# Optimization experiments

Measured on AMD Instinct MI355X. Metric: run time of the kernel, lower is better.

The kernel has to match this reference:

```python
import jax, jax.numpy as jnp
import numpy as np

D_MODEL = 1024
N_HEADS = 16
HEAD_DIM = D_MODEL // N_HEADS
B, LQ, LK = 4, 2048, 2048


def _rope(x, cos, sin):
    # x: (B, H, L, d); cos/sin: (B, 1, L, d)
    d = x.shape[-1]
    x1, x2 = x[..., : d // 2], x[..., d // 2 :]
    rotated = jnp.concatenate([-x2, x1], axis=-1)
    return x * cos + rotated * sin


def setup_inputs() -> dict:
    key = jax.random.key(0)
    ks = jax.random.split(key, 16)
    s = 1.0 / np.sqrt(D_MODEL)
    inp = {
        "query": jax.random.normal(ks[0], (B, LQ, D_MODEL), jnp.float32),
        "key": jax.random.normal(ks[1], (B, LK, D_MODEL), jnp.float32),
        "value": jax.random.normal(ks[2], (B, LK, D_MODEL), jnp.float32),
        "cos_q": jax.random.normal(ks[3], (B, LQ, HEAD_DIM), jnp.float32),
        "sin_q": jax.random.normal(ks[4], (B, LQ, HEAD_DIM), jnp.float32),
        "cos_k": jax.random.normal(ks[5], (B, LK, HEAD_DIM), jnp.float32),
        "sin_k": jax.random.normal(ks[6], (B, LK, HEAD_DIM), jnp.float32),
        "key_padding_mask": jnp.zeros((B, LK), dtype=bool),
        "Wq": jax.random.normal(ks[7], (D_MODEL, D_MODEL), jnp.float32) * s,
        "bq": jnp.zeros((D_MODEL,), jnp.float32),
        "Wk": jax.random.normal(ks[8], (D_MODEL, D_MODEL), jnp.float32) * s,
        "bk": jnp.zeros((D_MODEL,), jnp.float32),
        "Wv": jax.random.normal(ks[9], (D_MODEL, D_MODEL), jnp.float32) * s,
        "bv": jnp.zeros((D_MODEL,), jnp.float32),
        "Wo": jax.random.normal(ks[10], (D_MODEL, D_MODEL), jnp.float32) * s,
        "bo": jnp.zeros((D_MODEL,), jnp.float32),
    }
    return inp


def reference(query, key, value, cos_q, sin_q, cos_k, sin_k, key_padding_mask,
              Wq, bq, Wk, bk, Wv, bv, Wo, bo):
    Bq, Lq, _ = query.shape
    Lk = key.shape[1]
    scale = HEAD_DIM ** -0.5

    def proj(x, W, b, L):
        # torch Linear: x @ W.T + b, then (B, L, H, d) -> (B, H, L, d)
        y = jnp.einsum('ble,de->bld', x, W) + b
        return y.reshape(Bq, L, N_HEADS, HEAD_DIM).transpose(0, 2, 1, 3)

    q = proj(query, Wq, bq, Lq)
    k = proj(key, Wk, bk, Lk)
    v = proj(value, Wv, bv, Lk)

    q = _rope(q, cos_q[:, None, :Lq, :HEAD_DIM], sin_q[:, None, :Lq, :HEAD_DIM])
    k = _rope(k, cos_k[:, None, :Lk, :HEAD_DIM], sin_k[:, None, :Lk, :HEAD_DIM])

    attn = jnp.einsum('bhqd,bhkd->bhqk', q, k) * scale
    attn = jnp.where(key_padding_mask[:, None, None, :], -jnp.inf, attn)
    attn = jax.nn.softmax(attn, axis=-1)

    out = jnp.einsum('bhqk,bhkd->bhqd', attn, v)
    out = out.transpose(0, 2, 1, 3).reshape(Bq, Lq, D_MODEL)
    return jnp.einsum('ble,de->bld', out, Wo) + bo
```

## Files before the change

kernel.cpp:

```cpp
#include <hip/hip_runtime.h>
#include <hip/hip_bf16.h>
#include <stdint.h>
#include <stddef.h>

#define B_DIM 4
#define NH    16
#define LSEQ  2048
#define HD    64
#define DM    1024
#define TOKENS (B_DIM * LSEQ)

typedef __bf16 bf16_t;
typedef __attribute__((ext_vector_type(8))) __bf16 bf16x8;
typedef __attribute__((ext_vector_type(4))) __bf16 bf16x4;
typedef __attribute__((ext_vector_type(4))) float  f32x4;

#define GLD16(gp, lp) \
  __builtin_amdgcn_global_load_lds((__attribute__((address_space(1))) void*)(gp), \
                                   (__attribute__((address_space(3))) void*)(lp), 16, 0, 0)

__device__ __forceinline__ f32x4 mfma_16x16x32(bf16x8 a, bf16x8 b, f32x4 c) {
  return __builtin_amdgcn_mfma_f32_16x16x32_bf16(a, b, c, 0, 0, 0);
}

__global__ __launch_bounds__(256) void cast3_kernel(const float* __restrict__ a,
                                                    const float* __restrict__ b,
                                                    const float* __restrict__ c,
                                                    bf16_t* __restrict__ dst, int n) {
  const float* src = (blockIdx.y == 0) ? a : (blockIdx.y == 1) ? b : c;
  const int i = (blockIdx.x * 256 + threadIdx.x) * 4;
  if (i < n) {
    const float4 v = *(const float4*)(src + i);
    bf16x4 o;
    o[0] = (bf16_t)v.x; o[1] = (bf16_t)v.y; o[2] = (bf16_t)v.z; o[3] = (bf16_t)v.w;
    *(bf16x4*)(dst + (size_t)blockIdx.y * n + i) = o;
  }
}

__global__ __launch_bounds__(256) void cast4_kernel(const float* __restrict__ a,
                                                    const float* __restrict__ b,
                                                    const float* __restrict__ c,
                                                    const float* __restrict__ d,
                                                    bf16_t* __restrict__ dst, int n) {
  const float* src = (blockIdx.y == 0) ? a : (blockIdx.y == 1) ? b
                   : (blockIdx.y == 2) ? c : d;
  const int i = (blockIdx.x * 256 + threadIdx.x) * 4;
  if (i < n) {
    const float4 v = *(const float4*)(src + i);
    bf16x4 o;
    o[0] = (bf16_t)v.x; o[1] = (bf16_t)v.y; o[2] = (bf16_t)v.z; o[3] = (bf16_t)v.w;
    *(bf16x4*)(dst + (size_t)blockIdx.y * n + i) = o;
  }
}

__global__ __launch_bounds__(256) void qkv_proj_kernel(const bf16_t* __restrict__ X,
                                                       const bf16_t* __restrict__ Wb,
                                                       const float* __restrict__ bq,
                                                       const float* __restrict__ bk,
                                                       const float* __restrict__ bv,
                                                       const float* __restrict__ cos_q,
                                                       const float* __restrict__ sin_q,
                                                       const float* __restrict__ cos_k,
                                                       const float* __restrict__ sin_k,
                                                       bf16_t* __restrict__ qtb,
                                                       bf16_t* __restrict__ ktb,
                                                       bf16_t* __restrict__ vtb) {
  __shared__ bf16_t As[128 * 32];
  __shared__ bf16_t Bs[128 * 32];
  const int z = blockIdx.z;
  const bf16_t* A  = X  + (size_t)z * TOKENS * DM;
  const bf16_t* Bw = Wb + (size_t)z * DM * DM;
  const float* bias = (z == 0) ? bq : (z == 1) ? bk : bv;

  const int tid  = threadIdx.x;
  const int wave = tid >> 6, lane = tid & 63;
  const int quad = lane >> 4, l16 = lane & 15;
  const int m0 = blockIdx.x * 128, n0 = blockIdx.y * 128;
  const int wm = (wave >> 1) * 64, wn = (wave & 1) * 64;

  f32x4 acc[4][4];
#pragma unroll
  for (int i = 0; i < 4; ++i)
#pragma unroll
    for (int j = 0; j < 4; ++j) acc[i][j] = (f32x4){0.f, 0.f, 0.f, 0.f};

  const int srow = lane >> 2;
  const int scol = (lane & 3) * 8;

  for (int kk = 0; kk < DM; kk += 32) {
    __syncthreads();
#pragma unroll
    for (int t = 0; t < 2; ++t) {
      const int c   = wave * 2 + t;
      const int row = c * 16 + srow;
      GLD16(A  + (size_t)(m0 + row) * DM + kk + scol, As + c * 512);
      GLD16(Bw + (size_t)(n0 + row) * DM + kk + scol, Bs + c * 512);
    }
    __syncthreads();
    bf16x8 af[4], bfr[4];
#pragma unroll
    for (int i = 0; i < 4; ++i)
      af[i] = *(const bf16x8*)(As + (wm + i * 16 + l16) * 32 + quad * 8);
#pragma unroll
    for (int j = 0; j < 4; ++j)
      bfr[j] = *(const bf16x8*)(Bs + (wn + j * 16 + l16) * 32 + quad * 8);
#pragma unroll
    for (int i = 0; i < 4; ++i)
#pragma unroll
      for (int j = 0; j < 4; ++j)
        acc[i][j] = mfma_16x16x32(af[i], bfr[j], acc[i][j]);
  }

  if (z < 2) {
    const float* cosb = (z == 0) ? cos_q : cos_k;
    const float* sinb = (z == 0) ? sin_q : sin_k;
    bf16_t* out = (z == 0) ? qtb : ktb;
    const int h = (n0 + wn) >> 6;
#pragma unroll
    for (int i = 0; i < 4; ++i) {
#pragma unroll
      for (int j = 0; j < 2; ++j) {
        const int hd1 = j * 16 + l16;
        const int hd2 = hd1 + 32;
        const float bn1 = bias[n0 + wn + hd1];
        const float bn2 = bias[n0 + wn + hd2];
#pragma unroll
        for (int r = 0; r < 4; ++r) {
          const int m = m0 + wm + i * 16 + quad * 4 + r;
          const int b = m >> 11, l = m & (LSEQ - 1);
          const size_t cb = ((size_t)b * LSEQ + l) * HD;
          const float x1 = (float)(bf16_t)(acc[i][j][r] + bn1);
          const float x2 = (float)(bf16_t)(acc[i][j + 2][r] + bn2);
          const float c1 = cosb[cb + hd1], s1 = sinb[cb + hd1];
          const float c2 = cosb[cb + hd2], s2 = sinb[cb + hd2];
          bf16_t* dst = out + (((size_t)(b * NH + h)) * LSEQ + l) * HD;
          dst[hd1] = (bf16_t)(x1 * c1 - x2 * s1);
          dst[hd2] = (bf16_t)(x2 * c2 + x1 * s2);
        }
      }
    }
  } else {
#pragma unroll
    for (int i = 0; i < 4; ++i) {
      const int mb = m0 + wm + i * 16 + quad * 4;
      const int b = mb >> 11, l = mb & (LSEQ - 1);
#pragma unroll
      for (int j = 0; j < 4; ++j) {
        const int n = n0 + wn + j * 16 + l16;
        const int h = n >> 6, hd = n & (HD - 1);
        const float bn = bias[n];
        bf16x4 pk;
#pragma unroll
        for (int r = 0; r < 4; ++r) pk[r] = (bf16_t)(acc[i][j][r] + bn);
        *(bf16x4*)(vtb + (((size_t)(b * NH + h)) * HD + hd) * LSEQ + l) = pk;
      }
    }
  }
}

__global__ __launch_bounds__(256) void out_gemm_kernel(const bf16_t* __restrict__ A,
                                                       const bf16_t* __restrict__ Bw,
                                                       const float* __restrict__ bias,
                                                       float* __restrict__ out) {
  __shared__ bf16_t As[128 * 32];
  __shared__ bf16_t Bs[128 * 32];
  const int tid  = threadIdx.x;
  const int wave = tid >> 6, lane = tid & 63;
  const int quad = lane >> 4, l16 = lane & 15;
  const int m0 = blockIdx.x * 128, n0 = blockIdx.y * 128;
  const int wm = (wave >> 1) * 64, wn = (wave & 1) * 64;

  f32x4 acc[4][4];
#pragma unroll
  for (int i = 0; i < 4; ++i)
#pragma unroll
    for (int j = 0; j < 4; ++j) acc[i][j] = (f32x4){0.f, 0.f, 0.f, 0.f};

  const int srow = lane >> 2;
  const int scol = (lane & 3) * 8;

  for (int kk = 0; kk < DM; kk += 32) {
    __syncthreads();
#pragma unroll
    for (int t = 0; t < 2; ++t) {
      const int c   = wave * 2 + t;
      const int row = c * 16 + srow;
      GLD16(A  + (size_t)(m0 + row) * DM + kk + scol, As + c * 512);
      GLD16(Bw + (size_t)(n0 + row) * DM + kk + scol, Bs + c * 512);
    }
    __syncthreads();
    bf16x8 af[4], bfr[4];
#pragma unroll
    for (int i = 0; i < 4; ++i)
      af[i] = *(const bf16x8*)(As + (wm + i * 16 + l16) * 32 + quad * 8);
#pragma unroll
    for (int j = 0; j < 4; ++j)
      bfr[j] = *(const bf16x8*)(Bs + (wn + j * 16 + l16) * 32 + quad * 8);
#pragma unroll
    for (int i = 0; i < 4; ++i)
#pragma unroll
      for (int j = 0; j < 4; ++j)
        acc[i][j] = mfma_16x16x32(af[i], bfr[j], acc[i][j]);
  }

#pragma unroll
  for (int i = 0; i < 4; ++i)
#pragma unroll
    for (int j = 0; j < 4; ++j) {
      const int n  = n0 + wn + j * 16 + l16;
      const float bn = bias[n];
#pragma unroll
      for (int r = 0; r < 4; ++r) {
        const int m = m0 + wm + i * 16 + quad * 4 + r;
        out[(size_t)m * DM + n] = acc[i][j][r] + bn;
      }
    }
}

__global__ __launch_bounds__(256) void attn_kernel(const bf16_t* __restrict__ qt,
                                                   const bf16_t* __restrict__ kt,
                                                   const bf16_t* __restrict__ vt,
                                                   const unsigned char* __restrict__ mask,
                                                   bf16_t* __restrict__ ctx) {
  __shared__ bf16_t Kl[64 * 64];
  __shared__ bf16_t Vl[64 * 64];
  __shared__ bf16_t Pl[4 * 16 * 72];
  const int bh = blockIdx.y;
  const int b = bh >> 4, h = bh & (NH - 1);
  const int q0 = blockIdx.x * 128;
  const int tid = threadIdx.x;
  const int wave = tid >> 6, lane = tid & 63;
  const int quad = lane >> 4, l16 = lane & 15;
  const float scale_l2e = 0.125f * 1.44269504f;

  bf16x8 qa[2][2];
#pragma unroll
  for (int u = 0; u < 2; ++u) {
    const bf16_t* qrow = qt + (((size_t)bh * LSEQ) + q0 + wave * 32 + u * 16 + l16) * HD;
    qa[u][0] = *(const bf16x8*)(qrow + quad * 8);
    qa[u][1] = *(const bf16x8*)(qrow + 32 + quad * 8);
  }

  f32x4 O[2][4];
  float l_part[2][4];
#pragma unroll
  for (int u = 0; u < 2; ++u)
#pragma unroll
    for (int j = 0; j < 4; ++j) { O[u][j] = (f32x4){0.f, 0.f, 0.f, 0.f}; l_part[u][j] = 0.f; }

  const bf16_t* kbase = kt + (size_t)bh * LSEQ * HD;
  const bf16_t* vbase = vt + (size_t)bh * HD * LSEQ;
  const unsigned char* mrow = mask + (size_t)b * LSEQ;

  const int srow = lane >> 3;
  const int scb  = lane & 7;
  bf16_t* Plw = Pl + wave * 16 * 72;

  for (int k0 = 0; k0 < LSEQ; k0 += 64) {
    __syncthreads();
#pragma unroll
    for (int t = 0; t < 2; ++t) {
      const int c   = wave * 2 + t;
      const int row = c * 8 + srow;
      const int gcb = scb ^ (row & 7);
      GLD16(kbase + (size_t)(k0 + row) * HD + gcb * 8, Kl + c * 512);
      GLD16(vbase + (size_t)row * LSEQ + k0 + gcb * 8, Vl + c * 512);
    }
    __syncthreads();

    float mb[4];
#pragma unroll
    for (int j = 0; j < 4; ++j)
      mb[j] = mrow[k0 + j * 16 + l16] ? -__builtin_inff() : 0.f;

    f32x4 S[2][4];
#pragma unroll
    for (int j = 0; j < 4; ++j) {
      const int row = j * 16 + l16;
      const int sw  = row & 7;
      const bf16x8 kb0 = *(const bf16x8*)(Kl + row * 64 + ((quad)     ^ sw) * 8);
      const bf16x8 kb1 = *(const bf16x8*)(Kl + row * 64 + ((quad + 4) ^ sw) * 8);
#pragma unroll
      for (int u = 0; u < 2; ++u) {
        f32x4 a = (f32x4){0.f, 0.f, 0.f, 0.f};
        a = mfma_16x16x32(qa[u][0], kb0, a);
        a = mfma_16x16x32(qa[u][1], kb1, a);
#pragma unroll
        for (int r = 0; r < 4; ++r) {
          const float e = __builtin_amdgcn_exp2f(fmaf(a[r], scale_l2e, mb[j]));
          S[u][j][r] = e;
          l_part[u][r] += e;
        }
      }
    }

    bf16x8 pa[2][2];
#pragma unroll
    for (int u = 0; u < 2; ++u) {
#pragma unroll
      for (int j = 0; j < 4; ++j)
#pragma unroll
        for (int r = 0; r < 4; ++r)
          Plw[(quad * 4 + r) * 72 + j * 16 + l16] = (bf16_t)S[u][j][r];
      pa[u][0] = *(const bf16x8*)(Plw + l16 * 72 + quad * 8);
      pa[u][1] = *(const bf16x8*)(Plw + l16 * 72 + 32 + quad * 8);
    }

#pragma unroll
    for (int jd = 0; jd < 4; ++jd) {
      const int vrow = jd * 16 + l16;
      const int sw   = vrow & 7;
      const bf16x8 vb0 = *(const bf16x8*)(Vl + vrow * 64 + ((quad)     ^ sw) * 8);
      const bf16x8 vb1 = *(const bf16x8*)(Vl + vrow * 64 + ((quad + 4) ^ sw) * 8);
#pragma unroll
      for (int u = 0; u < 2; ++u) {
        O[u][jd] = mfma_16x16x32(pa[u][0], vb0, O[u][jd]);
        O[u][jd] = mfma_16x16x32(pa[u][1], vb1, O[u][jd]);
      }
    }
  }

#pragma unroll
  for (int u = 0; u < 2; ++u)
#pragma unroll
    for (int r = 0; r < 4; ++r) {
      float s = l_part[u][r];
#pragma unroll
      for (int off = 1; off < 16; off <<= 1) s += __shfl_xor(s, off);
      l_part[u][r] = 1.0f / s;
    }

#pragma unroll
  for (int u = 0; u < 2; ++u)
#pragma unroll
    for (int jd = 0; jd < 4; ++jd)
#pragma unroll
      for (int r = 0; r < 4; ++r) {
        const int l = q0 + wave * 32 + u * 16 + quad * 4 + r;
        const int d = h * HD + jd * 16 + l16;
        const float o = O[u][jd][r] * l_part[u][r];
        ctx[((size_t)b * LSEQ + l) * DM + d] = (bf16_t)o;
      }
}

extern "C" void kernel_launch(void* const* d_in, const int* in_sizes, int n_in,
                              void* d_out, int out_size, void* d_ws, size_t ws_size,
                              hipStream_t stream) {
  (void)in_sizes; (void)n_in; (void)out_size; (void)ws_size;
  const float* query = (const float*)d_in[0];
  const float* key   = (const float*)d_in[1];
  const float* value = (const float*)d_in[2];
  const float* cos_q = (const float*)d_in[3];
  const float* sin_q = (const float*)d_in[4];
  const float* cos_k = (const float*)d_in[5];
  const float* sin_k = (const float*)d_in[6];
  const unsigned char* mask = (const unsigned char*)d_in[7];
  const float* Wq = (const float*)d_in[8];
  const float* bq = (const float*)d_in[9];
  const float* Wk = (const float*)d_in[10];
  const float* bk = (const float*)d_in[11];
  const float* Wv = (const float*)d_in[12];
  const float* bv = (const float*)d_in[13];
  const float* Wo = (const float*)d_in[14];
  const float* bo = (const float*)d_in[15];
  float* out = (float*)d_out;

  const size_t ACT = (size_t)TOKENS * DM;
  const size_t WEL = (size_t)DM * DM;

  bf16_t* p   = (bf16_t*)d_ws;
  bf16_t* xq  = p; p += ACT;
  bf16_t* xk  = p; p += ACT;
  bf16_t* xv  = p; p += ACT;
  bf16_t* wqb = p; p += WEL;
  bf16_t* wkb = p; p += WEL;
  bf16_t* wvb = p; p += WEL;
  bf16_t* wob = p; p += WEL;
  bf16_t* qtb = p; p += ACT;
  bf16_t* ktb = p; p += ACT;
  bf16_t* vtb = p; p += ACT;
  bf16_t* ctx = xk;
  (void)xv; (void)wkb; (void)wvb;

  cast3_kernel<<<dim3((int)(ACT / 1024), 3), 256, 0, stream>>>(query, key, value, xq, (int)ACT);
  cast4_kernel<<<dim3((int)(WEL / 1024), 4), 256, 0, stream>>>(Wq, Wk, Wv, Wo, wqb, (int)WEL);

  qkv_proj_kernel<<<dim3(TOKENS / 128, DM / 128, 3), 256, 0, stream>>>(
      xq, wqb, bq, bk, bv, cos_q, sin_q, cos_k, sin_k, qtb, ktb, vtb);

  attn_kernel<<<dim3(LSEQ / 128, B_DIM * NH), 256, 0, stream>>>(qtb, ktb, vtb, mask, ctx);

  out_gemm_kernel<<<dim3(TOKENS / 128, DM / 128), 256, 0, stream>>>(ctx, wob, bo, out);
}
```

Before: 392.6 us.

## Double-buffer K/V tiles and keep softmax probabilities in registers

The attention kernel now double-buffers the K and V tiles in shared memory, prefetching the next tile while the current one is computed, so each step needs one barrier instead of two. It swaps the MFMA operand order so the score tile comes out transposed, and permutes the K rows on load so the probabilities can be packed straight into the PV operand without a round trip through shared memory. The mask becomes a wave-uniform check that is skipped when a 64-key tile has no masked keys, and the row-sum reduction is simplified. The extra buffer doubles the K/V shared-memory footprint and the occupancy hint adds register pressure.

```diff
diff --git a/kernel.cpp b/kernel.cpp
--- a/kernel.cpp
+++ b/kernel.cpp
@@ -217,14 +217,13 @@
     }
 }
 
-__global__ __launch_bounds__(256) void attn_kernel(const bf16_t* __restrict__ qt,
-                                                   const bf16_t* __restrict__ kt,
-                                                   const bf16_t* __restrict__ vt,
-                                                   const unsigned char* __restrict__ mask,
-                                                   bf16_t* __restrict__ ctx) {
-  __shared__ bf16_t Kl[64 * 64];
-  __shared__ bf16_t Vl[64 * 64];
-  __shared__ bf16_t Pl[4 * 16 * 72];
+__global__ __launch_bounds__(256, 4) void attn_kernel(const bf16_t* __restrict__ qt,
+                                                      const bf16_t* __restrict__ kt,
+                                                      const bf16_t* __restrict__ vt,
+                                                      const unsigned char* __restrict__ mask,
+                                                      bf16_t* __restrict__ ctx) {
+  __shared__ bf16_t Kl[2][64 * 64];
+  __shared__ bf16_t Vl[2][64 * 64];
   const int bh = blockIdx.y;
   const int b = bh >> 4, h = bh & (NH - 1);
   const int q0 = blockIdx.x * 128;
@@ -242,93 +241,128 @@
   }
 
   f32x4 O[2][4];
-  float l_part[2][4];
+  float l_part[2] = {0.f, 0.f};
 #pragma unroll
   for (int u = 0; u < 2; ++u)
 #pragma unroll
-    for (int j = 0; j < 4; ++j) { O[u][j] = (f32x4){0.f, 0.f, 0.f, 0.f}; l_part[u][j] = 0.f; }
+    for (int j = 0; j < 4; ++j) O[u][j] = (f32x4){0.f, 0.f, 0.f, 0.f};
 
   const bf16_t* kbase = kt + (size_t)bh * LSEQ * HD;
   const bf16_t* vbase = vt + (size_t)bh * HD * LSEQ;
   const unsigned char* mrow = mask + (size_t)b * LSEQ;
 
-  const int srow = lane >> 3;
-  const int scb  = lane & 7;
-  bf16_t* Plw = Pl + wave * 16 * 72;
-
-  for (int k0 = 0; k0 < LSEQ; k0 += 64) {
-    __syncthreads();
-#pragma unroll
-    for (int t = 0; t < 2; ++t) {
-      const int c   = wave * 2 + t;
-      const int row = c * 8 + srow;
-      const int gcb = scb ^ (row & 7);
-      GLD16(kbase + (size_t)(k0 + row) * HD + gcb * 8, Kl + c * 512);
-      GLD16(vbase + (size_t)row * LSEQ + k0 + gcb * 8, Vl + c * 512);
-    }
-    __syncthreads();
-
-    float mb[4];
-#pragma unroll
-    for (int j = 0; j < 4; ++j)
-      mb[j] = mrow[k0 + j * 16 + l16] ? -__builtin_inff() : 0.f;
+  const int srow8 = lane >> 3;
+  const int scb   = lane & 7;
+
+#pragma unroll
+  for (int tt = 0; tt < 2; ++tt) {
+    const int c = wave * 2 + tt;
+    const int p = c * 8 + srow8;
+    const int gcb = scb ^ (p & 7);
+    const int sig = ((p >> 5) << 5) | (((p >> 2) & 3) << 3) | (((p >> 4) & 1) << 2) | (p & 3);
+    GLD16(kbase + (size_t)sig * HD + gcb * 8, &Kl[0][0] + c * 512);
+    GLD16(vbase + (size_t)p * LSEQ + gcb * 8, &Vl[0][0] + c * 512);
+  }
+  __syncthreads();
+
+  int cur = 0;
+  for (int t = 0; t < 32; ++t) {
+    const int k0 = t * 64;
+
+    if (t < 31) {
+      const int k0n = k0 + 64;
+      bf16_t* Kd = &Kl[cur ^ 1][0];
+      bf16_t* Vd = &Vl[cur ^ 1][0];
+#pragma unroll
+      for (int tt = 0; tt < 2; ++tt) {
+        const int c = wave * 2 + tt;
+        const int p = c * 8 + srow8;
+        const int gcb = scb ^ (p & 7);
+        const int sig = ((p >> 5) << 5) | (((p >> 2) & 3) << 3) | (((p >> 4) & 1) << 2) | (p & 3);
+        GLD16(kbase + (size_t)(k0n + sig) * HD + gcb * 8, Kd + c * 512);
+        GLD16(vbase + (size_t)p * LSEQ + k0n + gcb * 8, Vd + c * 512);
+      }
+    }
+
+    const bf16_t* Kc = &Kl[cur][0];
+    const bf16_t* Vc = &Vl[cur][0];
+
+    const uint64_t mlo = *(const uint64_t*)(mrow + k0 + quad * 8);
+    const uint64_t mhi = *(const uint64_t*)(mrow + k0 + 32 + quad * 8);
 
     f32x4 S[2][4];
 #pragma unroll
     for (int j = 0; j < 4; ++j) {
       const int row = j * 16 + l16;
       const int sw  = row & 7;
-      const bf16x8 kb0 = *(const bf16x8*)(Kl + row * 64 + ((quad)     ^ sw) * 8);
-      const bf16x8 kb1 = *(const bf16x8*)(Kl + row * 64 + ((quad + 4) ^ sw) * 8);
+      const bf16x8 kb0 = *(const bf16x8*)(Kc + row * 64 + ((quad)     ^ sw) * 8);
+      const bf16x8 kb1 = *(const bf16x8*)(Kc + row * 64 + ((quad + 4) ^ sw) * 8);
 #pragma unroll
       for (int u = 0; u < 2; ++u) {
         f32x4 a = (f32x4){0.f, 0.f, 0.f, 0.f};
-        a = mfma_16x16x32(qa[u][0], kb0, a);
-        a = mfma_16x16x32(qa[u][1], kb1, a);
-#pragma unroll
-        for (int r = 0; r < 4; ++r) {
-          const float e = __builtin_amdgcn_exp2f(fmaf(a[r], scale_l2e, mb[j]));
-          S[u][j][r] = e;
-          l_part[u][r] += e;
-        }
+        a = mfma_16x16x32(kb0, qa[u][0], a);
+        a = mfma_16x16x32(kb1, qa[u][1], a);
+#pragma unroll
+        for (int r = 0; r < 4; ++r)
+          S[u][j][r] = __builtin_amdgcn_exp2f(a[r] * scale_l2e);
+      }
+    }
+
+    if (!__all((mlo | mhi) == 0)) {
+#pragma unroll
+      for (int j = 0; j < 4; ++j) {
+        const uint64_t mm = (j & 2) ? mhi : mlo;
+#pragma unroll
+        for (int r = 0; r < 4; ++r)
+          if ((mm >> (((j & 1) * 4 + r) * 8)) & 0xff) {
+            S[0][j][r] = 0.f;
+            S[1][j][r] = 0.f;
+          }
       }
     }
 
     bf16x8 pa[2][2];
 #pragma unroll
     for (int u = 0; u < 2; ++u) {
+      float s = 0.f;
 #pragma unroll
       for (int j = 0; j < 4; ++j)
-#pragma unroll
-        for (int r = 0; r < 4; ++r)
-          Plw[(quad * 4 + r) * 72 + j * 16 + l16] = (bf16_t)S[u][j][r];
-      pa[u][0] = *(const bf16x8*)(Plw + l16 * 72 + quad * 8);
-      pa[u][1] = *(const bf16x8*)(Plw + l16 * 72 + 32 + quad * 8);
+        s += (S[u][j][0] + S[u][j][1]) + (S[u][j][2] + S[u][j][3]);
+      l_part[u] += s;
+#pragma unroll
+      for (int f = 0; f < 2; ++f)
+#pragma unroll
+        for (int e = 0; e < 8; ++e)
+          pa[u][f][e] = (bf16_t)S[u][2 * f + (e >> 2)][e & 3];
     }
 
 #pragma unroll
     for (int jd = 0; jd < 4; ++jd) {
       const int vrow = jd * 16 + l16;
       const int sw   = vrow & 7;
-      const bf16x8 vb0 = *(const bf16x8*)(Vl + vrow * 64 + ((quad)     ^ sw) * 8);
-      const bf16x8 vb1 = *(const bf16x8*)(Vl + vrow * 64 + ((quad + 4) ^ sw) * 8);
+      const bf16x8 vb0 = *(const bf16x8*)(Vc + vrow * 64 + ((quad)     ^ sw) * 8);
+      const bf16x8 vb1 = *(const bf16x8*)(Vc + vrow * 64 + ((quad + 4) ^ sw) * 8);
 #pragma unroll
       for (int u = 0; u < 2; ++u) {
         O[u][jd] = mfma_16x16x32(pa[u][0], vb0, O[u][jd]);
         O[u][jd] = mfma_16x16x32(pa[u][1], vb1, O[u][jd]);
       }
     }
-  }
-
-#pragma unroll
-  for (int u = 0; u < 2; ++u)
-#pragma unroll
-    for (int r = 0; r < 4; ++r) {
-      float s = l_part[u][r];
-#pragma unroll
-      for (int off = 1; off < 16; off <<= 1) s += __shfl_xor(s, off);
-      l_part[u][r] = 1.0f / s;
-    }
+
+    if (t < 31) __syncthreads();
+    cur ^= 1;
+  }
+
+  float linv[2][4];
+#pragma unroll
+  for (int u = 0; u < 2; ++u) {
+    float s = l_part[u];
+    s += __shfl_xor(s, 16);
+    s += __shfl_xor(s, 32);
+#pragma unroll
+    for (int r = 0; r < 4; ++r)
+      linv[u][r] = 1.0f / __shfl(s, quad * 4 + r);
+  }
 
 #pragma unroll
   for (int u = 0; u < 2; ++u)
@@ -338,7 +372,7 @@
       for (int r = 0; r < 4; ++r) {
         const int l = q0 + wave * 32 + u * 16 + quad * 4 + r;
         const int d = h * HD + jd * 16 + l16;
-        const float o = O[u][jd][r] * l_part[u][r];
+        const float o = O[u][jd][r] * linv[u][r];
         ctx[((size_t)b * LSEQ + l) * DM + d] = (bf16_t)o;
       }
 }
```

Measured after the change: 369.5 us. 5.9% less time.
